# Kernel optimization log

Hardware: AMD Instinct MI355X
Metric: run time of the kernel (lower is better)

## Reference

```python
import jax, jax.numpy as jnp
import numpy as np

B, C, V = 1024, 512, 256  # batch, num_conjunctions, num_variables


def setup_inputs() -> dict:
    key = jax.random.key(0)
    k1, k2, k3 = jax.random.split(key, 3)
    x0 = jax.random.uniform(k1, (B, V), dtype=jnp.float32)
    # torch init: conj = 1 - 2*rand  -> uniform in (-1, 1)
    conjunctions = 1.0 - 2.0 * jax.random.uniform(k2, (C, 2 * V), dtype=jnp.float32)
    # rw = 10 - 20*rand -> uniform in (-10, 10)
    rule_weights = 10.0 - 20.0 * jax.random.uniform(k3, (C,), dtype=jnp.float32)
    return {"x0": x0, "conjunctions": conjunctions, "rule_weights": rule_weights}


def reference(x0, conjunctions, rule_weights):
    mu = jax.nn.sigmoid(conjunctions)            # (C, 2V)
    x = jnp.concatenate((x0, 1.0 - x0), axis=1)  # (B, 2V)
    # fuzzy-AND: broadcast mul-add then min over literal axis
    x_pot = mu[None, :, :] * x[:, None, :] + (1.0 - mu)[None, :, :]  # (B, C, 2V)
    fit = jnp.min(x_pot, axis=-1)                # (B, C)
    return 5.0 + jnp.sum(rule_weights * fit, axis=-1)  # (B,)
```

## Files before the change

### kernel.cpp

```cpp
#include <hip/hip_runtime.h>


#define B_    1024
#define C_    512
#define V_    256
#define TWOV  512

#define BPB    8
#define NBG    (B_ / BPB)
#define NCH    4
#define WAVES  8

__global__ __launch_bounds__(256) void k_prep(const float* __restrict__ conj,
                                              float2* __restrict__ muT2,
                                              float* __restrict__ out) {
    const int c = blockIdx.x;
    const int v = threadIdx.x;
    if (c < 4) out[c * 256 + v] = 5.0f;
    float z1 = conj[(size_t)c * TWOV + v];
    float z2 = conj[(size_t)c * TWOV + V_ + v];
    float m1 = 1.0f / (1.0f + __expf(-z1));
    float m2 = 1.0f / (1.0f + __expf(-z2));
    muT2[(size_t)(v >> 1) * (2 * C_) + c * 2 + (v & 1)] = make_float2(m1, m2);
}

__global__ __launch_bounds__(512, 4) void k_main(const float* __restrict__ x0,
                                                 const float4* __restrict__ muT4,
                                                 const float* __restrict__ rw,
                                                 float* __restrict__ out) {
    const int tid    = threadIdx.x;
    const int lane   = tid & 63;
    const int wave_u = __builtin_amdgcn_readfirstlane(tid >> 6);
    const int t      = wave_u & 1;
    const int s      = wave_u >> 1;
    const int bg     = blockIdx.x;
    const int chunk  = blockIdx.y;
    const int c      = chunk * 128 + t * 64 + lane;
    const int v0     = s * 64;

    const float* xb = x0 + (size_t)bg * BPB * V_ + v0;

    const float4* mu1p = muT4 + (size_t)(v0 >> 1) * C_ + c;
    const float4* mu2p = mu1p + C_;

    const float rwc = rw[c];

    float m[BPB];
#pragma unroll
    for (int i = 0; i < BPB; ++i) m[i] = 0.0f;

    float4 XA0, XA1, XA2, XA3, XA4, XA5, XA6, XA7;
    float4 XB0, XB1, XB2, XB3, XB4, XB5, XB6, XB7;
    float4 ma0, mb0, ma1, mb1;

#define XL(X, q) do { \
    X##0 = *reinterpret_cast<const float4*>(xb + 0 * V_ + 4 * (q)); \
    X##1 = *reinterpret_cast<const float4*>(xb + 1 * V_ + 4 * (q)); \
    X##2 = *reinterpret_cast<const float4*>(xb + 2 * V_ + 4 * (q)); \
    X##3 = *reinterpret_cast<const float4*>(xb + 3 * V_ + 4 * (q)); \
    X##4 = *reinterpret_cast<const float4*>(xb + 4 * V_ + 4 * (q)); \
    X##5 = *reinterpret_cast<const float4*>(xb + 5 * V_ + 4 * (q)); \
    X##6 = *reinterpret_cast<const float4*>(xb + 6 * V_ + 4 * (q)); \
    X##7 = *reinterpret_cast<const float4*>(xb + 7 * V_ + 4 * (q)); \
} while (0)

#define MUL_NEXT(MA, MB) do { \
    MA = mu1p[0]; MB = mu2p[0]; mu1p += 2 * C_; mu2p += 2 * C_; \
} while (0)

#define PINM(MA, MB) \
    asm volatile("" : "+v"(MA.x), "+v"(MA.y), "+v"(MA.z), "+v"(MA.w), \
                      "+v"(MB.x), "+v"(MB.y), "+v"(MB.z), "+v"(MB.w))

#define CB(XV, MA, MB, bi) do { \
    float mm = m[bi]; \
    mm = fmaxf(fmaxf(__builtin_fmaf(-(MA).x, (XV).x, (MA).x), (MA).y * (XV).x), mm); \
    mm = fmaxf(fmaxf(__builtin_fmaf(-(MA).z, (XV).y, (MA).z), (MA).w * (XV).y), mm); \
    mm = fmaxf(fmaxf(__builtin_fmaf(-(MB).x, (XV).z, (MB).x), (MB).y * (XV).z), mm); \
    mm = fmaxf(fmaxf(__builtin_fmaf(-(MB).z, (XV).w, (MB).z), (MB).w * (XV).w), mm); \
    m[bi] = mm; } while (0)

#define COMPUTE(X, MA, MB) do { \
    CB(X##0, MA, MB, 0); CB(X##1, MA, MB, 1); \
    CB(X##2, MA, MB, 2); CB(X##3, MA, MB, 3); \
    CB(X##4, MA, MB, 4); CB(X##5, MA, MB, 5); \
    CB(X##6, MA, MB, 6); CB(X##7, MA, MB, 7); } while (0)

    XL(XA, 0);
    MUL_NEXT(ma0, mb0);

#define QSTEP(q, XC, XN, MAC, MBC, MAN, MBN) do { \
    XL(XN, (q) + 1);               \
    MUL_NEXT(MAN, MBN);            \
    PINM(MAC, MBC);                \
    COMPUTE(XC, MAC, MBC); } while (0)

    QSTEP( 0, XA, XB, ma0, mb0, ma1, mb1);
    QSTEP( 1, XB, XA, ma1, mb1, ma0, mb0);
    QSTEP( 2, XA, XB, ma0, mb0, ma1, mb1);
    QSTEP( 3, XB, XA, ma1, mb1, ma0, mb0);
    QSTEP( 4, XA, XB, ma0, mb0, ma1, mb1);
    QSTEP( 5, XB, XA, ma1, mb1, ma0, mb0);
    QSTEP( 6, XA, XB, ma0, mb0, ma1, mb1);
    QSTEP( 7, XB, XA, ma1, mb1, ma0, mb0);
    QSTEP( 8, XA, XB, ma0, mb0, ma1, mb1);
    QSTEP( 9, XB, XA, ma1, mb1, ma0, mb0);
    QSTEP(10, XA, XB, ma0, mb0, ma1, mb1);
    QSTEP(11, XB, XA, ma1, mb1, ma0, mb0);
    QSTEP(12, XA, XB, ma0, mb0, ma1, mb1);
    QSTEP(13, XB, XA, ma1, mb1, ma0, mb0);
    QSTEP(14, XA, XB, ma0, mb0, ma1, mb1);
    PINM(ma1, mb1);
    COMPUTE(XB, ma1, mb1);

#undef QSTEP
#undef COMPUTE
#undef CB
#undef PINM
#undef MUL_NEXT
#undef XL

    __shared__ float red[4 * 128 * 9];
    const int ci = t * 64 + lane;
#pragma unroll
    for (int bi = 0; bi < BPB; ++bi)
        red[(s * 128 + ci) * 9 + bi] = m[bi];
    __syncthreads();

    if (wave_u < 2) {
        float con0, con1, con2, con3, con4, con5, con6, con7;
#define FIN(bi, CON) do { \
        float mm = red[(0 * 128 + ci) * 9 + bi]; \
        mm = fmaxf(mm, red[(1 * 128 + ci) * 9 + bi]); \
        mm = fmaxf(mm, red[(2 * 128 + ci) * 9 + bi]); \
        mm = fmaxf(mm, red[(3 * 128 + ci) * 9 + bi]); \
        float v = rwc * (1.0f - mm); \
        v += __shfl_xor(v, 1, 64);  v += __shfl_xor(v, 2, 64); \
        v += __shfl_xor(v, 4, 64);  v += __shfl_xor(v, 8, 64); \
        v += __shfl_xor(v, 16, 64); v += __shfl_xor(v, 32, 64); \
        CON = v; } while (0)
        FIN(0, con0); FIN(1, con1); FIN(2, con2); FIN(3, con3);
        FIN(4, con4); FIN(5, con5); FIN(6, con6); FIN(7, con7);
#undef FIN
        float t0 = (lane & 1) ? con1 : con0;
        float t1 = (lane & 1) ? con3 : con2;
        float t2 = (lane & 1) ? con5 : con4;
        float t3 = (lane & 1) ? con7 : con6;
        float u0 = (lane & 2) ? t1 : t0;
        float u1 = (lane & 2) ? t3 : t2;
        float sel = (lane & 4) ? u1 : u0;
        if (lane < 8)
            atomicAdd(&out[bg * BPB + lane], sel);
    }
}

__global__ __launch_bounds__(256) void k_naive(const float* __restrict__ x0,
                                               const float* __restrict__ conj,
                                               const float* __restrict__ rw,
                                               float* __restrict__ out) {
    int b = blockIdx.x;
    int t = threadIdx.x;
    __shared__ float red[256];
    float acc = 0.0f;
    for (int c = t; c < C_; c += 256) {
        float m = 0.0f;
        for (int v = 0; v < V_; ++v) {
            float mu1 = 1.0f / (1.0f + expf(-conj[(size_t)c * TWOV + v]));
            float mu2 = 1.0f / (1.0f + expf(-conj[(size_t)c * TWOV + V_ + v]));
            float x = x0[(size_t)b * V_ + v];
            m = fmaxf(m, fmaxf(mu1 * (1.0f - x), mu2 * x));
        }
        acc += rw[c] * (1.0f - m);
    }
    red[t] = acc;
    __syncthreads();
    for (int s = 128; s > 0; s >>= 1) {
        if (t < s) red[t] += red[t + s];
        __syncthreads();
    }
    if (t == 0) out[b] = 5.0f + red[0];
}

extern "C" void kernel_launch(void* const* d_in, const int* in_sizes, int n_in,
                              void* d_out, int out_size, void* d_ws, size_t ws_size,
                              hipStream_t stream) {
    const float* x0   = (const float*)d_in[0];
    const float* conj = (const float*)d_in[1];
    const float* rw   = (const float*)d_in[2];
    float* out = (float*)d_out;

    const size_t mu_floats = (size_t)(V_ / 2) * C_ * 4;
    const size_t need = mu_floats * sizeof(float);

    if (ws_size < need) {
        k_naive<<<B_, 256, 0, stream>>>(x0, conj, rw, out);
        return;
    }

    float4* muT4 = (float4*)d_ws;

    k_prep<<<C_, 256, 0, stream>>>(conj, (float2*)muT4, out);
    dim3 grid(NBG, NCH);
    k_main<<<grid, 512, 0, stream>>>(x0, muT4, rw, out);
}
```

Before: 22.02 us.

## Stage x tile in LDS and triple-buffer mu loads with inline asm waits

The block now loads its 8-row x0 tile into shared memory once and reads x values from LDS in the inner loop, instead of having every wave issue redundant global float4 loads for x. Mu values are fetched with inline-asm global_load_dwordx4 into a three-deep register rotation, with explicit s_waitcnt vmcnt counters so two loads stay in flight while one set is computed. This is meant to cut global load traffic and VGPR pressure from the x double buffers and to keep memory latency hidden. It adds a block barrier and LDS reads, and it relies on hand-written waitcnt values being correct, since the compiler cannot track loads issued through inline asm.

Result: slower. 22.67 us (+2.9%).

```diff
diff --git a/kernel.cpp b/kernel.cpp
--- a/kernel.cpp
+++ b/kernel.cpp
@@ -9,7 +9,8 @@
 #define BPB    8
 #define NBG    (B_ / BPB)
 #define NCH    4
-#define WAVES  8
+
+typedef float f32x4 __attribute__((ext_vector_type(4)));
 
 __global__ __launch_bounds__(256) void k_prep(const float* __restrict__ conj,
                                               float2* __restrict__ muT2,
@@ -25,109 +26,96 @@
 }
 
 __global__ __launch_bounds__(512, 4) void k_main(const float* __restrict__ x0,
-                                                 const float4* __restrict__ muT4,
+                                                 const f32x4* __restrict__ muT4,
                                                  const float* __restrict__ rw,
                                                  float* __restrict__ out) {
-    const int tid    = threadIdx.x;
-    const int lane   = tid & 63;
-    const int wave_u = __builtin_amdgcn_readfirstlane(tid >> 6);
-    const int t      = wave_u & 1;
-    const int s      = wave_u >> 1;
-    const int bg     = blockIdx.x;
-    const int chunk  = blockIdx.y;
-    const int c      = chunk * 128 + t * 64 + lane;
-    const int v0     = s * 64;
+    const int tid  = threadIdx.x;
+    const int lane = tid & 63;
+    const int wave = tid >> 6;
+    const int t    = wave & 1;
+    const int s    = wave >> 1;
+    const int bg   = blockIdx.x;
+    const int chunk= blockIdx.y;
+    const int c    = chunk * 128 + t * 64 + lane;
+    const int xq   = s * 16;
 
-    const float* xb = x0 + (size_t)bg * BPB * V_ + v0;
+    __shared__ f32x4 xs4[BPB * V_ / 4];
+    __shared__ float red[4 * 128 * 9];
 
-    const float4* mu1p = muT4 + (size_t)(v0 >> 1) * C_ + c;
-    const float4* mu2p = mu1p + C_;
+    {
+        const f32x4* xg = reinterpret_cast<const f32x4*>(x0 + (size_t)bg * BPB * V_);
+        xs4[tid] = xg[tid];
+    }
 
-    const float rwc = rw[c];
+    const f32x4* mu1p = muT4 + (size_t)(s * 32) * C_ + c;
+    const f32x4* mu2p = mu1p + C_;
 
     float m[BPB];
 #pragma unroll
     for (int i = 0; i < BPB; ++i) m[i] = 0.0f;
 
-    float4 XA0, XA1, XA2, XA3, XA4, XA5, XA6, XA7;
-    float4 XB0, XB1, XB2, XB3, XB4, XB5, XB6, XB7;
-    float4 ma0, mb0, ma1, mb1;
+    f32x4 A0, B0, A1, B1, A2, B2;
 
-#define XL(X, q) do { \
-    X##0 = *reinterpret_cast<const float4*>(xb + 0 * V_ + 4 * (q)); \
-    X##1 = *reinterpret_cast<const float4*>(xb + 1 * V_ + 4 * (q)); \
-    X##2 = *reinterpret_cast<const float4*>(xb + 2 * V_ + 4 * (q)); \
-    X##3 = *reinterpret_cast<const float4*>(xb + 3 * V_ + 4 * (q)); \
-    X##4 = *reinterpret_cast<const float4*>(xb + 4 * V_ + 4 * (q)); \
-    X##5 = *reinterpret_cast<const float4*>(xb + 5 * V_ + 4 * (q)); \
-    X##6 = *reinterpret_cast<const float4*>(xb + 6 * V_ + 4 * (q)); \
-    X##7 = *reinterpret_cast<const float4*>(xb + 7 * V_ + 4 * (q)); \
-} while (0)
+#define MULOAD(DST, PTR) \
+    asm volatile("global_load_dwordx4 %0, %1, off" : "=v"(DST) : "v"(PTR))
+#define ISSUE(MA, MB) do { \
+    MULOAD(MA, mu1p); MULOAD(MB, mu2p); \
+    mu1p += 2 * C_; mu2p += 2 * C_; } while (0)
 
-#define MUL_NEXT(MA, MB) do { \
-    MA = mu1p[0]; MB = mu2p[0]; mu1p += 2 * C_; mu2p += 2 * C_; \
-} while (0)
+    ISSUE(A0, B0);
+    ISSUE(A1, B1);
 
-#define PINM(MA, MB) \
-    asm volatile("" : "+v"(MA.x), "+v"(MA.y), "+v"(MA.z), "+v"(MA.w), \
-                      "+v"(MB.x), "+v"(MB.y), "+v"(MB.z), "+v"(MB.w))
+    __syncthreads();
 
-#define CB(XV, MA, MB, bi) do { \
-    float mm = m[bi]; \
-    mm = fmaxf(fmaxf(__builtin_fmaf(-(MA).x, (XV).x, (MA).x), (MA).y * (XV).x), mm); \
-    mm = fmaxf(fmaxf(__builtin_fmaf(-(MA).z, (XV).y, (MA).z), (MA).w * (XV).y), mm); \
-    mm = fmaxf(fmaxf(__builtin_fmaf(-(MB).x, (XV).z, (MB).x), (MB).y * (XV).z), mm); \
-    mm = fmaxf(fmaxf(__builtin_fmaf(-(MB).z, (XV).w, (MB).z), (MB).w * (XV).w), mm); \
-    m[bi] = mm; } while (0)
+#define COMPUTE(q, MA, MB) do { \
+    _Pragma("unroll") \
+    for (int bi = 0; bi < BPB; ++bi) { \
+        f32x4 xc = xs4[bi * 64 + xq + (q)]; \
+        float mm = m[bi]; \
+        mm = fmaxf(fmaxf(__builtin_fmaf(-MA.x, xc.x, MA.x), MA.y * xc.x), mm); \
+        mm = fmaxf(fmaxf(__builtin_fmaf(-MA.z, xc.y, MA.z), MA.w * xc.y), mm); \
+        mm = fmaxf(fmaxf(__builtin_fmaf(-MB.x, xc.z, MB.x), MB.y * xc.z), mm); \
+        mm = fmaxf(fmaxf(__builtin_fmaf(-MB.z, xc.w, MB.z), MB.w * xc.w), mm); \
+        m[bi] = mm; \
+    } } while (0)
 
-#define COMPUTE(X, MA, MB) do { \
-    CB(X##0, MA, MB, 0); CB(X##1, MA, MB, 1); \
-    CB(X##2, MA, MB, 2); CB(X##3, MA, MB, 3); \
-    CB(X##4, MA, MB, 4); CB(X##5, MA, MB, 5); \
-    CB(X##6, MA, MB, 6); CB(X##7, MA, MB, 7); } while (0)
+#define QSTEP(q, MAC, MBC, MAN, MBN) do { \
+    ISSUE(MAN, MBN); \
+    asm volatile("s_waitcnt vmcnt(4)" : "+v"(MAC), "+v"(MBC)); \
+    COMPUTE(q, MAC, MBC); } while (0)
 
-    XL(XA, 0);
-    MUL_NEXT(ma0, mb0);
-
-#define QSTEP(q, XC, XN, MAC, MBC, MAN, MBN) do { \
-    XL(XN, (q) + 1);               \
-    MUL_NEXT(MAN, MBN);            \
-    PINM(MAC, MBC);                \
-    COMPUTE(XC, MAC, MBC); } while (0)
-
-    QSTEP( 0, XA, XB, ma0, mb0, ma1, mb1);
-    QSTEP( 1, XB, XA, ma1, mb1, ma0, mb0);
-    QSTEP( 2, XA, XB, ma0, mb0, ma1, mb1);
-    QSTEP( 3, XB, XA, ma1, mb1, ma0, mb0);
-    QSTEP( 4, XA, XB, ma0, mb0, ma1, mb1);
-    QSTEP( 5, XB, XA, ma1, mb1, ma0, mb0);
-    QSTEP( 6, XA, XB, ma0, mb0, ma1, mb1);
-    QSTEP( 7, XB, XA, ma1, mb1, ma0, mb0);
-    QSTEP( 8, XA, XB, ma0, mb0, ma1, mb1);
-    QSTEP( 9, XB, XA, ma1, mb1, ma0, mb0);
-    QSTEP(10, XA, XB, ma0, mb0, ma1, mb1);
-    QSTEP(11, XB, XA, ma1, mb1, ma0, mb0);
-    QSTEP(12, XA, XB, ma0, mb0, ma1, mb1);
-    QSTEP(13, XB, XA, ma1, mb1, ma0, mb0);
-    QSTEP(14, XA, XB, ma0, mb0, ma1, mb1);
-    PINM(ma1, mb1);
-    COMPUTE(XB, ma1, mb1);
+    QSTEP( 0, A0, B0, A2, B2);
+    QSTEP( 1, A1, B1, A0, B0);
+    QSTEP( 2, A2, B2, A1, B1);
+    QSTEP( 3, A0, B0, A2, B2);
+    QSTEP( 4, A1, B1, A0, B0);
+    QSTEP( 5, A2, B2, A1, B1);
+    QSTEP( 6, A0, B0, A2, B2);
+    QSTEP( 7, A1, B1, A0, B0);
+    QSTEP( 8, A2, B2, A1, B1);
+    QSTEP( 9, A0, B0, A2, B2);
+    QSTEP(10, A1, B1, A0, B0);
+    QSTEP(11, A2, B2, A1, B1);
+    QSTEP(12, A0, B0, A2, B2);
+    QSTEP(13, A1, B1, A0, B0);
+    asm volatile("s_waitcnt vmcnt(2)" : "+v"(A2), "+v"(B2));
+    COMPUTE(14, A2, B2);
+    asm volatile("s_waitcnt vmcnt(0)" : "+v"(A0), "+v"(B0));
+    COMPUTE(15, A0, B0);
 
 #undef QSTEP
 #undef COMPUTE
-#undef CB
-#undef PINM
-#undef MUL_NEXT
-#undef XL
+#undef ISSUE
+#undef MULOAD
 
-    __shared__ float red[4 * 128 * 9];
     const int ci = t * 64 + lane;
 #pragma unroll
     for (int bi = 0; bi < BPB; ++bi)
         red[(s * 128 + ci) * 9 + bi] = m[bi];
     __syncthreads();
 
-    if (wave_u < 2) {
+    if (wave < 2) {
+        const float rwc = rw[c];
         float con0, con1, con2, con3, con4, con5, con6, con7;
 #define FIN(bi, CON) do { \
         float mm = red[(0 * 128 + ci) * 9 + bi]; \
@@ -163,14 +151,14 @@
     __shared__ float red[256];
     float acc = 0.0f;
     for (int c = t; c < C_; c += 256) {
-        float m = 0.0f;
+        float mm = 0.0f;
         for (int v = 0; v < V_; ++v) {
             float mu1 = 1.0f / (1.0f + expf(-conj[(size_t)c * TWOV + v]));
             float mu2 = 1.0f / (1.0f + expf(-conj[(size_t)c * TWOV + V_ + v]));
             float x = x0[(size_t)b * V_ + v];
-            m = fmaxf(m, fmaxf(mu1 * (1.0f - x), mu2 * x));
+            mm = fmaxf(mm, fmaxf(mu1 * (1.0f - x), mu2 * x));
         }
-        acc += rw[c] * (1.0f - m);
+        acc += rw[c] * (1.0f - mm);
     }
     red[t] = acc;
     __syncthreads();
@@ -197,7 +185,7 @@
         return;
     }
 
-    float4* muT4 = (float4*)d_ws;
+    f32x4* muT4 = (f32x4*)d_ws;
 
     k_prep<<<C_, 256, 0, stream>>>(conj, (float2*)muT4, out);
     dim3 grid(NBG, NCH);
```
